# Kernel tuning notes

Hardware: AMD Instinct MI355X
Metric: run time of the kernel (lower is better)

The kernel has to match this reference:

```python
import jax, jax.numpy as jnp
import numpy as np

IMG = 224   # img_size
K = 8       # num_bands
E = 256     # embed_dim


def _radial_masks(size, k):
    # Faithful to torch _create_radial_masks: center = size//2, max_r = size/sqrt(2)
    center = size // 2
    y, x = jnp.meshgrid(jnp.arange(size), jnp.arange(size), indexing='ij')
    r = jnp.sqrt(((x - center) ** 2 + (y - center) ** 2).astype(jnp.float32))
    max_r = size / np.sqrt(2.0)
    step = np.float32(max_r / k)
    i = jnp.arange(k, dtype=jnp.float32)[:, None, None]
    masks = ((r[None] >= step * i) & (r[None] < step * (i + 1.0))).astype(jnp.float32)
    return masks  # [K, H, W]


def setup_inputs() -> dict:
    key = jax.random.key(0)
    ks = jax.random.split(key, 3)
    x = jax.random.normal(ks[0], (64, 3, IMG, IMG), dtype=jnp.float32)
    W1 = jax.random.normal(ks[1], (3, E), dtype=jnp.float32) * 0.3
    b1 = jnp.zeros((E,), jnp.float32)
    gamma = jnp.ones((E,), jnp.float32)
    beta = jnp.zeros((E,), jnp.float32)
    W2 = jax.random.normal(ks[2], (E, E), dtype=jnp.float32) * (1.0 / np.sqrt(E))
    b2 = jnp.zeros((E,), jnp.float32)
    return {"x": x, "W1": W1, "b1": b1, "gamma": gamma, "beta": beta, "W2": W2, "b2": b2}


def reference(x, W1, b1, gamma, beta, W2, b2):
    masks = _radial_masks(IMG, K)                    # [K,H,W], binary, non-overlapping
    x_gray = x.mean(axis=1)                          # [B,H,W]
    fft = jnp.fft.fftshift(jnp.fft.fft2(x_gray), axes=(-2, -1))
    mag = jnp.log1p(jnp.abs(fft))                    # log(1+|F|)
    mu = mag.mean(axis=(1, 2), keepdims=True)
    sd = jnp.std(mag, axis=(1, 2), keepdims=True, ddof=1) + 1e-6  # torch .std is unbiased
    magn = (mag - mu) / sd                           # [B,H,W]

    msum = masks.sum(axis=(1, 2))                    # [K], true mask pixel counts
    mask_sums = msum + 1e-6
    s1 = jnp.einsum('bhw,khw->bk', magn, masks)      # per-band sum
    s2 = jnp.einsum('bhw,khw->bk', magn * magn, masks)
    means = s1 / mask_sums
    # sum((magn - means)^2 * mask) = s2 - 2*means*s1 + means^2 * msum  (exact expansion)
    var_num = s2 - 2.0 * means * s1 + (means ** 2) * msum
    stds = jnp.sqrt(var_num / mask_sums + 1e-6)
    # masked_fill(mask==0, -1e9) then amax over H,W
    maxs = jnp.max(jnp.where(masks[None] > 0, magn[:, None], -1e9), axis=(2, 3))

    feats = jnp.stack([means, stds, maxs], axis=-1)  # [B,K,3]
    h = feats @ W1 + b1                              # [B,K,E]
    hm = h.mean(axis=-1, keepdims=True)
    hv = h.var(axis=-1, keepdims=True)
    h = (h - hm) / jnp.sqrt(hv + 1e-5) * gamma + beta  # LayerNorm, eps=1e-5
    h = jax.nn.relu(h)
    return h @ W2 + b2                               # [B,K,E]
```

## Files before the change

### kernel.cpp

```cpp
#include <hip/hip_runtime.h>
#include <math.h>

#define IMG 224
#define NPIX 50176
#define BATCH 64
#define EDIM 256

typedef _Float16 f16;
typedef __attribute__((ext_vector_type(8))) _Float16 f16x8;
typedef __attribute__((ext_vector_type(4))) _Float16 f16x4;
typedef __attribute__((ext_vector_type(4))) float f32x4;
typedef unsigned int u32;


#define GLD16(gp, lp)                                                          \
  __builtin_amdgcn_global_load_lds(                                            \
      (const __attribute__((address_space(1))) u32*)(gp),                      \
      (__attribute__((address_space(3))) u32*)(lp), 16, 0, 0)

template <int LDK, int NT>
__device__ __forceinline__ void gemm_core(const f16* __restrict__ A,
                                          const f16* __restrict__ B,
                                          int m0, int n0,
                                          f16 (*As)[64][64], f16 (*Bs)[128][64],
                                          f32x4 acc[2][4]) {
  int tid = threadIdx.x;
  int lane = tid & 63, wid = tid >> 6;
  int wr = wid >> 1, wc = wid & 1;
  int srow = lane >> 3;
  int sk8 = (lane & 7) ^ srow;

  auto stage = [&](int bufi, int t) {
    int k0 = t * 64;
#pragma unroll
    for (int ci = 0; ci < 6; ++ci) {
      int c = wid * 6 + ci;
      if (c < 8) {
        GLD16(A + (size_t)(m0 + c * 8 + srow) * LDK + k0 + sk8 * 8,
              &As[bufi][0][0] + c * 512);
      } else {
        int j = c - 8;
        GLD16(B + (size_t)(n0 + j * 8 + srow) * LDK + k0 + sk8 * 8,
              &Bs[bufi][0][0] + j * 512);
      }
    }
  };

  stage(0, 0);
#pragma unroll 1
  for (int t = 0; t < NT; ++t) {
    int cur = t & 1;
    if (t + 1 < NT) {
      stage(cur ^ 1, t + 1);
      asm volatile("s_waitcnt vmcnt(6)" ::: "memory");
    } else {
      asm volatile("s_waitcnt vmcnt(0)" ::: "memory");
    }
    __builtin_amdgcn_s_barrier();
#pragma unroll
    for (int kk = 0; kk < 2; ++kk) {
      f16x8 af[2], bfr[4];
#pragma unroll
      for (int mi = 0; mi < 2; ++mi) {
        int row = wr * 32 + mi * 16 + (lane & 15);
        int slot = (kk * 4 + (lane >> 4)) ^ (row & 7);
        af[mi] = *(const f16x8*)&As[cur][row][slot * 8];
      }
#pragma unroll
      for (int nj = 0; nj < 4; ++nj) {
        int row = wc * 64 + nj * 16 + (lane & 15);
        int slot = (kk * 4 + (lane >> 4)) ^ (row & 7);
        bfr[nj] = *(const f16x8*)&Bs[cur][row][slot * 8];
      }
#pragma unroll
      for (int mi = 0; mi < 2; ++mi)
#pragma unroll
        for (int nj = 0; nj < 4; ++nj)
          acc[mi][nj] = __builtin_amdgcn_mfma_f32_16x16x32_f16(
              af[mi], bfr[nj], acc[mi][nj], 0, 0, 0);
    }
    __builtin_amdgcn_s_barrier();
  }
}

__global__ __launch_bounds__(256) void gemmA_kernel(const f16* __restrict__ Gh,
                                                    const f16* __restrict__ B1,
                                                    f16* __restrict__ B2t) {
  __shared__ f16 As[2][64][64];
  __shared__ f16 Bs[2][128][64];
  int m0 = blockIdx.y * 64, n0 = blockIdx.x * 128;
  f32x4 acc[2][4];
#pragma unroll
  for (int i = 0; i < 2; ++i)
#pragma unroll
    for (int j = 0; j < 4; ++j) acc[i][j] = (f32x4){0.f, 0.f, 0.f, 0.f};

  gemm_core<256, 4>(Gh, B1, m0, n0, As, Bs, acc);

  int lane = threadIdx.x & 63, wid = threadIdx.x >> 6;
  int wr = wid >> 1, wc = wid & 1;
  int mbase = m0 + wr * 32, nbase = n0 + wc * 64;
#pragma unroll
  for (int mi = 0; mi < 2; ++mi) {
#pragma unroll
    for (int nj = 0; nj < 4; ++nj) {
      int c = nbase + nj * 16 + (lane & 15);
      if (c >= 226) continue;
      int m = mbase + mi * 16 + ((lane >> 4) << 2);
      int b = m / 224;
      int h = m - b * 224;
      int v = c, kb = h;
      if (c >= 113) { v = c - 113; kb = 224 + h; }
      size_t off = (size_t)(b * 128 + v) * 448 + kb;
      f32x4 y = acc[mi][nj];
      f16x4 hv;
#pragma unroll
      for (int r = 0; r < 4; ++r) hv[r] = (f16)y[r];
      *(f16x4*)&B2t[off] = hv;
    }
  }
}

__global__ __launch_bounds__(256) void gemmB_kernel(const f16* __restrict__ W2h,
                                                    const f16* __restrict__ B2t,
                                                    float* __restrict__ stats) {
  __shared__ f16 As[2][64][64];
  __shared__ f16 Bs[2][128][64];
  int b = blockIdx.x;
  int m0 = blockIdx.y * 64;
  f32x4 acc[2][4];
#pragma unroll
  for (int i = 0; i < 2; ++i)
#pragma unroll
    for (int j = 0; j < 4; ++j) acc[i][j] = (f32x4){0.f, 0.f, 0.f, 0.f};

  gemm_core<448, 7>(W2h, B2t + (size_t)b * 128 * 448, m0, 0, As, Bs, acc);

  int tid = threadIdx.x;
  int lane = tid & 63, wid = tid >> 6;
  int wr = wid >> 1, wc = wid & 1;
  int rbase = m0 + wr * 32;
  const float step = (float)(158.39191898578665 / 8.0);

  float gsum = 0.f, gsq = 0.f;
  float s1[8] = {0}, s2[8] = {0}, cnt[8] = {0};
  float mx[8] = {0, 0, 0, 0, 0, 0, 0, 0};

#pragma unroll
  for (int mi = 0; mi < 2; ++mi) {
#pragma unroll
    for (int nj = 0; nj < 4; ++nj) {
      int n = wc * 64 + nj * 16 + (lane & 15);
      if (n >= 113) continue;
      float wgt = (n >= 1 && n <= 111) ? 2.f : 1.f;
      float dx2 = (float)(n * n);
      int rr = rbase + mi * 16 + ((lane >> 4) << 2);
      f32x4 f = acc[mi][nj];
#pragma unroll
      for (int p = 0; p < 2; ++p) {
        int u = (rr >> 1) + p;
        float re = f[2 * p], im = f[2 * p + 1];
        float mv = log1pf(sqrtf(re * re + im * im));
        int a = (u <= 111) ? u : 224 - u;
        float r = sqrtf((float)(a * a) + dx2);
        int bd = 255;
#pragma unroll
        for (int k = 0; k < 8; k++) {
          float lo = step * (float)k;
          float hi = step * (float)(k + 1);
          if (r >= lo && r < hi) bd = k;
        }
        float wm = wgt * mv;
        gsum += wm;
        gsq += wm * mv;
#pragma unroll
        for (int k = 0; k < 8; k++) {
          bool m = (bd == k);
          s1[k] += m ? wm : 0.f;
          s2[k] += m ? wm * mv : 0.f;
          cnt[k] += m ? wgt : 0.f;
          mx[k] = m ? fmaxf(mx[k], mv) : mx[k];
        }
      }
    }
  }

  float vals[34];
  vals[0] = gsum; vals[1] = gsq;
#pragma unroll
  for (int k = 0; k < 8; k++) {
    vals[2 + k] = s1[k]; vals[10 + k] = s2[k]; vals[18 + k] = mx[k]; vals[26 + k] = cnt[k];
  }
#pragma unroll
  for (int i = 0; i < 34; i++) {
    float v = vals[i];
    const bool isMax = (i >= 18 && i < 26);
#pragma unroll
    for (int off = 32; off > 0; off >>= 1) {
      float o = __shfl_down(v, off);
      v = isMax ? fmaxf(v, o) : (v + o);
    }
    vals[i] = v;
  }
  float* red = (float*)&As[0][0][0];
  if ((tid & 63) == 0) {
#pragma unroll
    for (int i = 0; i < 34; i++) red[wid * 34 + i] = vals[i];
  }
  __syncthreads();
  if (tid < 34) {
    bool isMax = (tid >= 18 && tid < 26);
    float v = red[tid];
#pragma unroll
    for (int ww = 1; ww < 4; ww++) {
      float o = red[ww * 34 + tid];
      v = isMax ? fmaxf(v, o) : (v + o);
    }
    if (isMax)
      atomicMax((u32*)&stats[b * 34 + tid], __float_as_uint(v));
    else
      atomicAdd(&stats[b * 34 + tid], v);
  }
}

__global__ __launch_bounds__(256) void prep_kernel(const float* __restrict__ x,
                                                   f16* __restrict__ Gh,
                                                   f16* __restrict__ B1,
                                                   f16* __restrict__ W2h,
                                                   f16* __restrict__ B2t,
                                                   float* __restrict__ stats) {
  int blk = blockIdx.x;
  int tid = threadIdx.x;
  if (blk < 14336) {
    int m = blk, k = tid;
    float g = 0.f;
    if (k < 224) {
      int b = m / 224, h = m - b * 224;
      const float* xb = x + (size_t)b * 3 * NPIX + h * IMG + k;
      g = (xb[0] + xb[NPIX] + xb[2 * NPIX]) * (1.0f / 3.0f);
    }
    Gh[(size_t)m * 256 + k] = (f16)g;
  } else if (blk < 14592) {
    int n = blk - 14336, k = tid;
    float val = 0.f;
    if (k < 224 && n < 226) {
      int v = (n < 113) ? n : n - 113;
      int m = (k * v) % 224;
      float mf = (float)m / 112.0f;
      val = (n < 113) ? cospif(mf) : -sinpif(mf);
    }
    B1[n * 256 + k] = (f16)val;
  } else if (blk < 15376) {
    int i = (blk - 14592) * 256 + tid;
    int row = i / 448;
    int k = i - row * 448;
    int u = row >> 1;
    bool imrow = row & 1;
    bool kim = k >= 224;
    int kk = kim ? k - 224 : k;
    int m = (u * kk) % 224;
    float mf = (float)m / 112.0f;
    float c = cospif(mf), s = sinpif(mf);
    float val = imrow ? (kim ? c : -s) : (kim ? s : c);
    W2h[i] = (f16)val;
  } else if (blk < 16216) {
    int w = (blk - 15376) * 256 + tid;
    int img = w / 3360;
    int off = w - img * 3360;
    ((u32*)B2t)[(size_t)(img * 128 + 113) * 224 + off] = 0;
  } else {
    int i = (blk - 16216) * 256 + tid;
    if (i < BATCH * 34) stats[i] = 0.f;
  }
}

__global__ __launch_bounds__(256) void mlp_kernel(const float* __restrict__ stats,
                                                  const float* __restrict__ W1,
                                                  const float* __restrict__ b1,
                                                  const float* __restrict__ gamma,
                                                  const float* __restrict__ beta,
                                                  const float* __restrict__ W2m,
                                                  const float* __restrict__ b2,
                                                  float* __restrict__ out) {
  int bk = blockIdx.x;
  int b = bk >> 3, k = bk & 7;
  int e = threadIdx.x;

  __shared__ float st[34];
  if (e < 34) st[e] = stats[b * 34 + e];
  __syncthreads();

  const float N = (float)NPIX;
  float mu = st[0] / N;
  float varg = fmaxf(st[1] - N * mu * mu, 0.0f) / (N - 1.0f);
  float sd = sqrtf(varg) + 1e-6f;

  float s1r = st[2 + k], s2r = st[10 + k], mxr = st[18 + k], cntk = st[26 + k];
  float ms = cntk + 1e-6f;
  float s1n = (s1r - mu * cntk) / sd;
  float s2n = (s2r - 2.0f * mu * s1r + mu * mu * cntk) / (sd * sd);
  float mean_k = s1n / ms;
  float var_num = s2n - 2.0f * mean_k * s1n + mean_k * mean_k * cntk;
  float std_k = sqrtf(var_num / ms + 1e-6f);
  float max_k = (mxr - mu) / sd;

  float h = mean_k * W1[e] + std_k * W1[EDIM + e] + max_k * W1[2 * EDIM + e] + b1[e];

  float s = h, q = h * h;
#pragma unroll
  for (int off = 32; off > 0; off >>= 1) {
    s += __shfl_down(s, off);
    q += __shfl_down(q, off);
  }
  __shared__ float rs[4], rq[4];
  __shared__ float hmS, hvS;
  if ((e & 63) == 0) { rs[e >> 6] = s; rq[e >> 6] = q; }
  __syncthreads();
  if (e == 0) {
    float ts = rs[0] + rs[1] + rs[2] + rs[3];
    float tq = rq[0] + rq[1] + rq[2] + rq[3];
    float hm = ts / 256.0f;
    hmS = hm;
    hvS = fmaxf(tq / 256.0f - hm * hm, 0.0f);
  }
  __syncthreads();
  float hn = (h - hmS) / sqrtf(hvS + 1e-5f) * gamma[e] + beta[e];
  float hr = fmaxf(hn, 0.0f);

  __shared__ float hs[EDIM];
  hs[e] = hr;
  __syncthreads();

  float acc = b2[e];
#pragma unroll 8
  for (int j = 0; j < EDIM; j++) acc += hs[j] * W2m[j * EDIM + e];
  out[(size_t)bk * EDIM + e] = acc;
}

extern "C" void kernel_launch(void* const* d_in, const int* in_sizes, int n_in,
                              void* d_out, int out_size, void* d_ws, size_t ws_size,
                              hipStream_t stream) {
  const float* x     = (const float*)d_in[0];
  const float* W1    = (const float*)d_in[1];
  const float* b1    = (const float*)d_in[2];
  const float* gamma = (const float*)d_in[3];
  const float* beta  = (const float*)d_in[4];
  const float* W2m   = (const float*)d_in[5];
  const float* b2    = (const float*)d_in[6];
  float* out = (float*)d_out;

  char* W = (char*)d_ws;
  f16* Gh  = (f16*)W;
  f16* B2t = (f16*)(W + 7340032);
  f16* B1  = (f16*)(W + 14680064);
  f16* W2h = (f16*)(W + 14680064 + 131072);
  float* stats = (float*)(W + 14680064 + 131072 + 401408);

  prep_kernel<<<dim3(16225), dim3(256), 0, stream>>>(x, Gh, B1, W2h, B2t, stats);
  gemmA_kernel<<<dim3(2, 224), dim3(256), 0, stream>>>(Gh, B1, B2t);
  gemmB_kernel<<<dim3(BATCH, 7), dim3(256), 0, stream>>>(W2h, B2t, stats);
  mlp_kernel<<<dim3(BATCH * 8), dim3(256), 0, stream>>>(stats, W1, b1, gamma, beta, W2m, b2, out);
}
```

Measured before the change: 54.53 us.

## Fuse grayscale conversion into first DFT GEMM and widen its N tile

The grayscale averaging and fp16 conversion move out of the prep kernel into the first GEMM's A-tile loader. The GEMM now reads the three fp32 channels directly into registers, averages them and writes swizzled fp16 to LDS. This removes the 7 MB Gh intermediate write and its re-read. Each block now covers the full 256-wide N dimension, so x is read once, at the cost of more accumulator registers, a larger B LDS buffer and half as many blocks.

Result: slower. 56.54 us (+3.7%).

```diff
diff --git a/kernel.cpp b/kernel.cpp
--- a/kernel.cpp
+++ b/kernel.cpp
@@ -17,6 +17,133 @@
   __builtin_amdgcn_global_load_lds(                                            \
       (const __attribute__((address_space(1))) u32*)(gp),                      \
       (__attribute__((address_space(3))) u32*)(lp), 16, 0, 0)
+
+__global__ __launch_bounds__(256) void gemmA_kernel(const float* __restrict__ x,
+                                                    const f16* __restrict__ B1,
+                                                    f16* __restrict__ B2t) {
+  __shared__ f16 As[2][64][64];
+  __shared__ f16 Bs[2][256][64];
+  int m0 = blockIdx.x * 64;
+  int tid = threadIdx.x;
+  int lane = tid & 63, wid = tid >> 6;
+  int wr = wid >> 1, wc = wid & 1;
+
+  int arow = tid >> 2;
+  int aseg = tid & 3;
+  int am = m0 + arow;
+  int ab = am / 224, ah = am - ab * 224;
+  const float* px = x + (size_t)ab * 3 * NPIX + ah * IMG;
+  int s0 = (aseg * 2) ^ (arow & 7);
+  int s1 = (aseg * 2 + 1) ^ (arow & 7);
+
+  int srow = lane >> 3;
+  int sk8 = (lane & 7) ^ srow;
+
+  f32x4 xl[3][4];
+
+  f32x4 acc[2][8];
+#pragma unroll
+  for (int i = 0; i < 2; ++i)
+#pragma unroll
+    for (int j = 0; j < 8; ++j) acc[i][j] = (f32x4){0.f, 0.f, 0.f, 0.f};
+
+  auto issueA = [&](int t) {
+    int kb = t * 64 + aseg * 16;
+    if (kb < 224) {
+#pragma unroll
+      for (int c = 0; c < 3; ++c)
+#pragma unroll
+        for (int q = 0; q < 4; ++q)
+          xl[c][q] = *(const f32x4*)(px + c * NPIX + kb + q * 4);
+    }
+  };
+  auto issueB = [&](int bufi, int t) {
+    int k0 = t * 64;
+#pragma unroll
+    for (int ci = 0; ci < 8; ++ci) {
+      int j = wid * 8 + ci;
+      GLD16(B1 + (size_t)(j * 8 + srow) * 256 + k0 + sk8 * 8,
+            &Bs[bufi][0][0] + j * 512);
+    }
+  };
+  auto writeA = [&](int bufi, int t) {
+    int kb = t * 64 + aseg * 16;
+    f16x8 h0, h1;
+    if (kb < 224) {
+#pragma unroll
+      for (int j = 0; j < 8; ++j) {
+        int q = j >> 2, r = j & 3;
+        h0[j] = (f16)((xl[0][q][r] + xl[1][q][r] + xl[2][q][r]) * (1.0f / 3.0f));
+      }
+#pragma unroll
+      for (int j = 0; j < 8; ++j) {
+        int q = 2 + (j >> 2), r = j & 3;
+        h1[j] = (f16)((xl[0][q][r] + xl[1][q][r] + xl[2][q][r]) * (1.0f / 3.0f));
+      }
+    } else {
+#pragma unroll
+      for (int j = 0; j < 8; ++j) { h0[j] = (f16)0.f; h1[j] = (f16)0.f; }
+    }
+    *(f16x8*)&As[bufi][arow][s0 * 8] = h0;
+    *(f16x8*)&As[bufi][arow][s1 * 8] = h1;
+  };
+
+  issueA(0);
+  issueB(0, 0);
+#pragma unroll 1
+  for (int t = 0; t < 4; ++t) {
+    int cur = t & 1;
+    asm volatile("s_waitcnt vmcnt(0)" ::: "memory");
+    writeA(cur, t);
+    asm volatile("s_waitcnt lgkmcnt(0)" ::: "memory");
+    __builtin_amdgcn_s_barrier();
+    if (t < 3) { issueA(t + 1); issueB(cur ^ 1, t + 1); }
+#pragma unroll
+    for (int kk = 0; kk < 2; ++kk) {
+      f16x8 af[2], bfr[8];
+#pragma unroll
+      for (int mi = 0; mi < 2; ++mi) {
+        int row = wr * 32 + mi * 16 + (lane & 15);
+        int slot = (kk * 4 + (lane >> 4)) ^ (row & 7);
+        af[mi] = *(const f16x8*)&As[cur][row][slot * 8];
+      }
+#pragma unroll
+      for (int nj = 0; nj < 8; ++nj) {
+        int row = wc * 128 + nj * 16 + (lane & 15);
+        int slot = (kk * 4 + (lane >> 4)) ^ (row & 7);
+        bfr[nj] = *(const f16x8*)&Bs[cur][row][slot * 8];
+      }
+#pragma unroll
+      for (int mi = 0; mi < 2; ++mi)
+#pragma unroll
+        for (int nj = 0; nj < 8; ++nj)
+          acc[mi][nj] = __builtin_amdgcn_mfma_f32_16x16x32_f16(
+              af[mi], bfr[nj], acc[mi][nj], 0, 0, 0);
+    }
+    __builtin_amdgcn_s_barrier();
+  }
+
+  int mbase = m0 + wr * 32, nbase = wc * 128;
+#pragma unroll
+  for (int mi = 0; mi < 2; ++mi) {
+#pragma unroll
+    for (int nj = 0; nj < 8; ++nj) {
+      int c = nbase + nj * 16 + (lane & 15);
+      if (c >= 226) continue;
+      int m = mbase + mi * 16 + ((lane >> 4) << 2);
+      int b = m / 224;
+      int h = m - b * 224;
+      int v = c, kb = h;
+      if (c >= 113) { v = c - 113; kb = 224 + h; }
+      size_t off = (size_t)(b * 128 + v) * 448 + kb;
+      f32x4 y = acc[mi][nj];
+      f16x4 hv;
+#pragma unroll
+      for (int r = 0; r < 4; ++r) hv[r] = (f16)y[r];
+      *(f16x4*)&B2t[off] = hv;
+    }
+  }
+}
 
 template <int LDK, int NT>
 __device__ __forceinline__ void gemm_core(const f16* __restrict__ A,
@@ -83,44 +210,6 @@
   }
 }
 
-__global__ __launch_bounds__(256) void gemmA_kernel(const f16* __restrict__ Gh,
-                                                    const f16* __restrict__ B1,
-                                                    f16* __restrict__ B2t) {
-  __shared__ f16 As[2][64][64];
-  __shared__ f16 Bs[2][128][64];
-  int m0 = blockIdx.y * 64, n0 = blockIdx.x * 128;
-  f32x4 acc[2][4];
-#pragma unroll
-  for (int i = 0; i < 2; ++i)
-#pragma unroll
-    for (int j = 0; j < 4; ++j) acc[i][j] = (f32x4){0.f, 0.f, 0.f, 0.f};
-
-  gemm_core<256, 4>(Gh, B1, m0, n0, As, Bs, acc);
-
-  int lane = threadIdx.x & 63, wid = threadIdx.x >> 6;
-  int wr = wid >> 1, wc = wid & 1;
-  int mbase = m0 + wr * 32, nbase = n0 + wc * 64;
-#pragma unroll
-  for (int mi = 0; mi < 2; ++mi) {
-#pragma unroll
-    for (int nj = 0; nj < 4; ++nj) {
-      int c = nbase + nj * 16 + (lane & 15);
-      if (c >= 226) continue;
-      int m = mbase + mi * 16 + ((lane >> 4) << 2);
-      int b = m / 224;
-      int h = m - b * 224;
-      int v = c, kb = h;
-      if (c >= 113) { v = c - 113; kb = 224 + h; }
-      size_t off = (size_t)(b * 128 + v) * 448 + kb;
-      f32x4 y = acc[mi][nj];
-      f16x4 hv;
-#pragma unroll
-      for (int r = 0; r < 4; ++r) hv[r] = (f16)y[r];
-      *(f16x4*)&B2t[off] = hv;
-    }
-  }
-}
-
 __global__ __launch_bounds__(256) void gemmB_kernel(const f16* __restrict__ W2h,
                                                     const f16* __restrict__ B2t,
                                                     float* __restrict__ stats) {
@@ -223,25 +312,14 @@
   }
 }
 
-__global__ __launch_bounds__(256) void prep_kernel(const float* __restrict__ x,
-                                                   f16* __restrict__ Gh,
-                                                   f16* __restrict__ B1,
+__global__ __launch_bounds__(256) void prep_kernel(f16* __restrict__ B1,
                                                    f16* __restrict__ W2h,
                                                    f16* __restrict__ B2t,
                                                    float* __restrict__ stats) {
   int blk = blockIdx.x;
   int tid = threadIdx.x;
-  if (blk < 14336) {
-    int m = blk, k = tid;
-    float g = 0.f;
-    if (k < 224) {
-      int b = m / 224, h = m - b * 224;
-      const float* xb = x + (size_t)b * 3 * NPIX + h * IMG + k;
-      g = (xb[0] + xb[NPIX] + xb[2 * NPIX]) * (1.0f / 3.0f);
-    }
-    Gh[(size_t)m * 256 + k] = (f16)g;
-  } else if (blk < 14592) {
-    int n = blk - 14336, k = tid;
+  if (blk < 256) {
+    int n = blk, k = tid;
     float val = 0.f;
     if (k < 224 && n < 226) {
       int v = (n < 113) ? n : n - 113;
@@ -250,8 +328,8 @@
       val = (n < 113) ? cospif(mf) : -sinpif(mf);
     }
     B1[n * 256 + k] = (f16)val;
-  } else if (blk < 15376) {
-    int i = (blk - 14592) * 256 + tid;
+  } else if (blk < 1040) {
+    int i = (blk - 256) * 256 + tid;
     int row = i / 448;
     int k = i - row * 448;
     int u = row >> 1;
@@ -263,13 +341,13 @@
     float c = cospif(mf), s = sinpif(mf);
     float val = imrow ? (kim ? c : -s) : (kim ? s : c);
     W2h[i] = (f16)val;
-  } else if (blk < 16216) {
-    int w = (blk - 15376) * 256 + tid;
+  } else if (blk < 1880) {
+    int w = (blk - 1040) * 256 + tid;
     int img = w / 3360;
     int off = w - img * 3360;
     ((u32*)B2t)[(size_t)(img * 128 + 113) * 224 + off] = 0;
   } else {
-    int i = (blk - 16216) * 256 + tid;
+    int i = (blk - 1880) * 256 + tid;
     if (i < BATCH * 34) stats[i] = 0.f;
   }
 }
@@ -350,14 +428,13 @@
   float* out = (float*)d_out;
 
   char* W = (char*)d_ws;
-  f16* Gh  = (f16*)W;
-  f16* B2t = (f16*)(W + 7340032);
-  f16* B1  = (f16*)(W + 14680064);
-  f16* W2h = (f16*)(W + 14680064 + 131072);
-  float* stats = (float*)(W + 14680064 + 131072 + 401408);
-
-  prep_kernel<<<dim3(16225), dim3(256), 0, stream>>>(x, Gh, B1, W2h, B2t, stats);
-  gemmA_kernel<<<dim3(2, 224), dim3(256), 0, stream>>>(Gh, B1, B2t);
+  f16* B2t = (f16*)W;
+  f16* B1  = (f16*)(W + 7340032);
+  f16* W2h = (f16*)(W + 7340032 + 131072);
+  float* stats = (float*)(W + 7340032 + 131072 + 401408);
+
+  prep_kernel<<<dim3(1889), dim3(256), 0, stream>>>(B1, W2h, B2t, stats);
+  gemmA_kernel<<<dim3(224), dim3(256), 0, stream>>>(x, B1, B2t);
   gemmB_kernel<<<dim3(BATCH, 7), dim3(256), 0, stream>>>(W2h, B2t, stats);
   mlp_kernel<<<dim3(BATCH * 8), dim3(256), 0, stream>>>(stats, W1, b1, gamma, beta, W2m, b2, out);
 }
```
